# Optimization experiments

Hardware: AMD Instinct MI355X
Metric: run time of the kernel (lower is better)

Reference implementation:

```python
import jax, jax.numpy as jnp
import numpy as np

B = 32768
ONE_STEP = 344  # 12*6 + 8*6 + 18*6 + 2+2+2 + 13 + 2+2 + 2 + 1 + 36 + 36 + 6+6+6


def _info(c):
    # c: [B, 344] one history step; slice per example_extend_info layout
    b = c.shape[0]
    return dict(
        hdv=c[:, 0:72].reshape(b, 12, 6),
        cav=c[:, 72:120].reshape(b, 8, 6),
        lane=c[:, 120:228].reshape(b, 18, 6),
        bott=c[:, 228:230], road_end=c[:, 230:232], target=c[:, 232:234],
        self_=c[:, 234:247].reshape(b, 1, 13),
        dist_bott=c[:, 247:249], dist_end=c[:, 249:251],
        exe=c[:, 251:253].reshape(b, 1, 2), gen=c[:, 253:254].reshape(b, 1, 1),
    )


def _star_mask(n):
    # adj = ones; adj[1:,1:] = 0  -> ego node 0 connected to everyone
    m = jnp.zeros((n, n), bool)
    return m.at[0, :].set(True).at[:, 0].set(True)


def _gat(x, adj, Wh, a1, a2, Wo, ao1, ao2):
    # pyGAT-style dense multi-head GAT (eval mode, dropout off), returns ego node feats
    h = jnp.einsum('bnf,hfo->bhno', x, Wh)                         # [B,H,N,16]
    e = jax.nn.leaky_relu(jnp.einsum('bhno,ho->bhn', h, a1)[:, :, :, None]
                          + jnp.einsum('bhno,ho->bhn', h, a2)[:, :, None, :], 0.2)
    att = jax.nn.softmax(jnp.where(adj[None, None], e, -9e15), axis=-1)
    h = jax.nn.elu(jnp.einsum('bhnm,bhmo->bhno', att, h))          # concat-head layer
    b, H, n, o = h.shape
    x2 = h.transpose(0, 2, 1, 3).reshape(b, n, H * o)              # [B,N,48]
    ho = x2 @ Wo                                                   # [B,N,64]
    e2 = jax.nn.leaky_relu((ho @ ao1)[:, :, None] + (ho @ ao2)[:, None, :], 0.2)
    att2 = jax.nn.softmax(jnp.where(adj[None], e2, -9e15), axis=-1)
    return jax.nn.elu(jnp.einsum('bnm,bmo->bno', att2, ho))[:, 0, :]


def _fwd(obs, W_self, b_self, W_dyn, b_dyn,
         hdv_Wh, hdv_a1, hdv_a2, hdv_Wo, hdv_ao1, hdv_ao2,
         cav_Wh, cav_a1, cav_a2, cav_Wo, cav_ao1, cav_ao2,
         lane_W1, lane_b1, lane_W2, lane_b2,
         comb_W1, comb_b1, comb_W2, comb_b2):
    b = obs.shape[0]
    # history chunks: [h5,h4,h3,h2,h1,current]; forward uses h4..current
    infos = [_info(obs[:, i * ONE_STEP:(i + 1) * ONE_STEP]) for i in (1, 2, 3, 4, 5)]
    cur = infos[-1]
    ego_hist = jnp.concatenate([inf['self_'][:, :, :3] for inf in infos], axis=2)  # [B,1,15]
    x = jax.nn.leaky_relu(ego_hist @ W_self + b_self, 0.1)[:, 0, :]                # squeeze(1)
    ego_feat = jax.nn.leaky_relu(x, 0.1) @ W_dyn + b_dyn                            # [B,64]
    ego3 = cur['self_'][:, :, :3]
    hdv_rel = _gat(jnp.concatenate([ego3, cur['hdv'][:, :, :3]], axis=1), _star_mask(13),
                   hdv_Wh, hdv_a1, hdv_a2, hdv_Wo, hdv_ao1, hdv_ao2)
    cav_rel = _gat(jnp.concatenate([ego3, cur['cav'][:, :, :3]], axis=1), _star_mask(9),
                   cav_Wh, cav_a1, cav_a2, cav_Wo, cav_ao1, cav_ao2)
    lane = jax.nn.relu(jax.nn.relu(cur['lane'].reshape(b, 108) @ lane_W1 + lane_b1) @ lane_W2 + lane_b2)
    road = jnp.concatenate([cur['bott'], cur['dist_bott'], cur['road_end'],
                            cur['dist_end'], cur['target']], axis=1)               # [B,10]
    comb = jnp.concatenate([ego_feat, hdv_rel, cav_rel, lane, road,
                            cur['gen'].reshape(b, 1), cur['exe'].reshape(b, 2)], axis=1)  # [B,269]
    return jax.nn.relu(jax.nn.relu(comb @ comb_W1 + comb_b1) @ comb_W2 + comb_b2)  # [B,64]


def setup_inputs() -> dict:
    ks = jax.random.split(jax.random.key(0), 24)
    def n(i, shape):
        return jax.random.normal(ks[i], shape, jnp.float32) * 0.1
    z = lambda s: jnp.zeros(s, jnp.float32)
    return {
        'obs': jax.random.normal(ks[0], (B, 6 * ONE_STEP), jnp.float32),
        'W_self': n(1, (15, 128)), 'b_self': z((128,)),
        'W_dyn': n(2, (128, 64)), 'b_dyn': z((64,)),
        'hdv_Wh': n(3, (3, 3, 16)), 'hdv_a1': n(4, (3, 16)), 'hdv_a2': n(5, (3, 16)),
        'hdv_Wo': n(6, (48, 64)), 'hdv_ao1': n(7, (64,)), 'hdv_ao2': n(8, (64,)),
        'cav_Wh': n(9, (3, 3, 16)), 'cav_a1': n(10, (3, 16)), 'cav_a2': n(11, (3, 16)),
        'cav_Wo': n(12, (48, 64)), 'cav_ao1': n(13, (64,)), 'cav_ao2': n(14, (64,)),
        'lane_W1': n(15, (108, 64)), 'lane_b1': z((64,)),
        'lane_W2': n(16, (64, 64)), 'lane_b2': z((64,)),
        'comb_W1': n(17, (269, 64)), 'comb_b1': z((64,)),
        'comb_W2': n(18, (64, 64)), 'comb_b2': z((64,)),
        'batch_size': B,
    }


def reference(obs, W_self, b_self, W_dyn, b_dyn,
              hdv_Wh, hdv_a1, hdv_a2, hdv_Wo, hdv_ao1, hdv_ao2,
              cav_Wh, cav_a1, cav_a2, cav_Wo, cav_ao1, cav_ao2,
              lane_W1, lane_b1, lane_W2, lane_b2,
              comb_W1, comb_b1, comb_W2, comb_b2, batch_size):
    return _fwd(obs, W_self, b_self, W_dyn, b_dyn,
                hdv_Wh, hdv_a1, hdv_a2, hdv_Wo, hdv_ao1, hdv_ao2,
                cav_Wh, cav_a1, cav_a2, cav_Wo, cav_ao1, cav_ao2,
                lane_W1, lane_b1, lane_W2, lane_b2,
                comb_W1, comb_b1, comb_W2, comb_b2)
```

## Files before the change

### kernel.cpp

```cpp
#include <hip/hip_runtime.h>
#include <math.h>

#define ROW 2064
#define OS  344

typedef _Float16 h2 __attribute__((ext_vector_type(2)));
typedef _Float16 h8 __attribute__((ext_vector_type(8)));

#define OFF_EGO 0
#define OFF_DYN 3072
#define OFF_L1  11264
#define OFF_L2  18432
#define OFF_WHX 22528
#define OFF_WO  22912
#define OFF_W1  29056
#define OFF_W2  47488
#define WT_F16  51584
#define FB_BSELF 0
#define FB_BDYN 128
#define FB_LB1 192
#define FB_LB2 256
#define FB_CB1 320
#define FB_CB2 384
#define FB_SU  448
#define FB_AO  484
#define FS_TOT 740

union U4 { uint4 q; h2 p[8]; };
union U1 { uint u; h2 h; };

__device__ __forceinline__ float fd(h2 a, h2 b, float c){
#if __has_builtin(__builtin_amdgcn_fdot2)
  return __builtin_amdgcn_fdot2(a,b,c,false);
#else
  return c + (float)a.x*(float)b.x + (float)a.y*(float)b.y;
#endif
}
__device__ __forceinline__ float lrelu(float x,float s){ return x>=0.f? x : s*x; }
__device__ __forceinline__ float eluf(float x){ return x>0.f? x : expm1f(x); }
__device__ __forceinline__ uint packh2(float a,float b){ U1 u; u.h=(h2){(_Float16)a,(_Float16)b}; return u.u; }

__device__ __forceinline__ int span_to_comb(int sp){
  switch(sp){ case 228: return 256; case 229: return 257; case 230: return 260; case 231: return 261;
    case 232: return 264; case 233: return 265; case 247: return 258; case 248: return 259;
    case 249: return 262; case 250: return 263; case 251: return 267; case 252: return 268;
    case 253: return 266; default: return -1; }
}

__global__ void k_prep(const float* __restrict__ Wself, const float* __restrict__ Wdyn,
                       const float* __restrict__ lW1, const float* __restrict__ lW2,
                       const float* __restrict__ hWh, const float* __restrict__ cWh,
                       const float* __restrict__ hWo, const float* __restrict__ cWo,
                       const float* __restrict__ ha1, const float* __restrict__ ha2,
                       const float* __restrict__ ca1, const float* __restrict__ ca2,
                       const float* __restrict__ hao1, const float* __restrict__ hao2,
                       const float* __restrict__ cao1, const float* __restrict__ cao2,
                       const float* __restrict__ bself, const float* __restrict__ bdyn,
                       const float* __restrict__ lb1, const float* __restrict__ lb2,
                       const float* __restrict__ cb1, const float* __restrict__ cb2,
                       _Float16* __restrict__ wt)
{
  int gid = blockIdx.x*blockDim.x + threadIdx.x;
  int nth = gridDim.x*blockDim.x;
  for (int idx = gid; idx < OFF_W1; idx += nth){
    float v = 0.f;
    if (idx < OFF_DYN){ int l=idx; int j=l/24, k=l%24;
      if (k<16){ int s=k>>2, c=k&3; if (c<3) v = Wself[(s*3+c)*128 + j]; }
      else { int sp = 232 + (k-16); if (sp>=234 && sp<=236) v = Wself[(12+(sp-234))*128 + j]; }
    } else if (idx < OFF_L1){ int l=idx-OFF_DYN; int j=l>>7, k=l&127; v = Wdyn[k*64+j]; }
    else if (idx < OFF_L2){ int l=idx-OFF_L1; int j=l/112, k=l%112; if (k<108) v = lW1[k*64+j]; }
    else if (idx < OFF_WHX){ int l=idx-OFF_L2; int j=l>>6, k=l&63; v = lW2[k*64+j]; }
    else if (idx < OFF_WO){ int l=idx-OFF_WHX; int g=l/192; l-=g*192; int j=l>>2, k=l&3;
      const float* Wh = g? cWh : hWh; int hh=j>>4, o=j&15; if (k<3) v = Wh[hh*48 + k*16 + o]; }
    else { int l=idx-OFF_WO; int g=l/3072; l-=g*3072; int j=l/48, k=l%48;
      const float* Wo = g? cWo : hWo; v = Wo[k*64+j]; }
    wt[idx] = (_Float16)v;
  }
  float* fso = (float*)(wt + WT_F16);
  for (int i = gid; i < FS_TOT; i += nth){
    float v=0.f;
    if (i<128) v = bself[i];
    else if (i<192) v = bdyn[i-128];
    else if (i<256) v = lb1[i-192];
    else if (i<320) v = lb2[i-256];
    else if (i<384) v = cb1[i-320];
    else if (i<448) v = cb2[i-384];
    else if (i<484){ int t=i-448; int g=t/18, w=(t%18)/9, hh=(t%9)/3, f=t%3;
      const float* A = g? (w? ca2:ca1) : (w? ha2:ha1);
      const float* WH = g? cWh : hWh; v=0.f;
      for (int o=0;o<16;++o) v += WH[hh*48+f*16+o]*A[hh*16+o]; }
    else { int t=i-484; int g=t>>7, w=(t>>6)&1, j=t&63;
      const float* A = g? (w?cao2:cao1) : (w?hao2:hao1); v = A[j]; }
    fso[i]=v;
  }
}

__global__ void k_prep2(const float* __restrict__ cmW1, const float* __restrict__ cmW2,
                        _Float16* __restrict__ wt)
{
  int gid = blockIdx.x*blockDim.x + threadIdx.x;
  int nth = gridDim.x*blockDim.x;
  for (int idx = gid + OFF_W1; idx < WT_F16; idx += nth){
    float v = 0.f;
    if (idx < OFF_W2){ int l=idx-OFF_W1; int j=l/288, k=l%288;
      int r = (k<256) ? k : span_to_comb(224 + (k-256));
      if (r>=0) v = cmW1[r*64 + j];
    } else { int l=idx-OFF_W2; int j=l>>6, k=l&63; v = cmW2[k*64+j]; }
    wt[idx] = (_Float16)v;
  }
}

__device__ __forceinline__ float dot8u(uint a,uint b,uint c,uint d, const U4& q, float t){
  U1 u; u.u=a; t=fd(u.h,q.p[0],t); u.u=b; t=fd(u.h,q.p[1],t);
  u.u=c; t=fd(u.h,q.p[2],t); u.u=d; t=fd(u.h,q.p[3],t); return t;
}

__device__ __forceinline__ void gpass8(float acc[8], const _Float16* xl,
    const _Float16* __restrict__ wt, long wbase, int KP, int C){
  #pragma unroll 2
  for (int c=0;c<C;++c){
    union{h8 v; uint u[4];} x; x.v = *(const h8*)(xl + (long)c*512);
    #pragma unroll
    for (int j=0;j<8;++j){
      U4 q = *(const U4*)(wt + wbase + (long)j*KP + c*8);
      acc[j] = dot8u(x.u[0],x.u[1],x.u[2],x.u[3],q,acc[j]);
    }
  }
}

__device__ __forceinline__ void put_piece(_Float16* pbase, int wj, int lane, const float* v8){
  uint4 q; q.x=packh2(v8[0],v8[1]); q.y=packh2(v8[2],v8[3]);
  q.z=packh2(v8[4],v8[5]); q.w=packh2(v8[6],v8[7]);
  *(uint4*)(pbase + wj*512 + lane*8) = q;
}

template<int N>
__device__ __forceinline__ void gat_phase1(const float* __restrict__ fs,
    const _Float16* __restrict__ wt, const float* __restrict__ nod,
    int g, int hh, _Float16* scr, int lane)
{
  const int xoff = (N==13)? 0 : 72;
  float sx0=nod[234], sy0=nod[235], sz0=nod[236];
  float u10=fs[FB_SU+g*18+hh*3+0], u11=fs[FB_SU+g*18+hh*3+1], u12=fs[FB_SU+g*18+hh*3+2];
  float u20=fs[FB_SU+g*18+9+hh*3+0], u21=fs[FB_SU+g*18+9+hh*3+1], u22=fs[FB_SU+g*18+9+hh*3+2];
  float s1v = u10*sx0 + u11*sy0 + u12*sz0;
  float sc[N]; float mx = -1e30f;
  #pragma unroll
  for (int n=0;n<N;++n){
    float nx,ny,nz;
    if (n==0){ nx=sx0; ny=sy0; nz=sz0; }
    else { int b0=xoff+(n-1)*6; nx=nod[b0]; ny=nod[b0+1]; nz=nod[b0+2]; }
    float ev = lrelu(s1v + u20*nx + u21*ny + u22*nz, 0.2f);
    sc[n]=ev; mx=fmaxf(mx,ev);
  }
  float sum=0.f;
  #pragma unroll
  for (int n=0;n<N;++n){ float w=__expf(sc[n]-mx); sc[n]=w; sum+=w; }
  float inv = 1.f/sum;
  float g0=0.f,g1=0.f,g2=0.f;
  #pragma unroll
  for (int n=0;n<N;++n){
    float a = sc[n]*inv; float nx,ny,nz;
    if (n==0){ nx=sx0; ny=sy0; nz=sz0; }
    else { int b0=xoff+(n-1)*6; nx=nod[b0]; ny=nod[b0+1]; nz=nod[b0+2]; }
    g0 += a*nx; g1 += a*ny; g2 += a*nz;
  }
  const _Float16* wh = wt + OFF_WHX + g*192 + (hh*16)*4;
  uint o20[8], o2X[8];
  #pragma unroll
  for (int t=0;t<8;++t){
    float wa0=(float)wh[(2*t)*4],   wa1=(float)wh[(2*t)*4+1],   wa2=(float)wh[(2*t)*4+2];
    float wb0=(float)wh[(2*t+1)*4], wb1=(float)wh[(2*t+1)*4+1], wb2=(float)wh[(2*t+1)*4+2];
    float v0 = eluf(g0*wa0 + g1*wa1 + g2*wa2);
    float v1 = eluf(g0*wb0 + g1*wb1 + g2*wb2);
    float xv0= eluf(sx0*wa0 + sy0*wa1 + sz0*wa2);
    float xv1= eluf(sx0*wb0 + sy0*wb1 + sz0*wb2);
    o20[t]=packh2(v0,v1); o2X[t]=packh2(xv0,xv1);
  }
  int c20 = (g*2)*6 + 2*hh, c2X = (g*2+1)*6 + 2*hh;
  *(uint4*)(scr + (long)c20*512 + lane*8)     = make_uint4(o20[0],o20[1],o20[2],o20[3]);
  *(uint4*)(scr + (long)(c20+1)*512 + lane*8) = make_uint4(o20[4],o20[5],o20[6],o20[7]);
  *(uint4*)(scr + (long)c2X*512 + lane*8)     = make_uint4(o2X[0],o2X[1],o2X[2],o2X[3]);
  *(uint4*)(scr + (long)(c2X+1)*512 + lane*8) = make_uint4(o2X[4],o2X[5],o2X[6],o2X[7]);
}

__global__ __launch_bounds__(512,4) void k_main(const float* __restrict__ obs,
    const _Float16* __restrict__ wt, float* __restrict__ out, int Bn)
{
  __shared__ __align__(16) unsigned char smem[60416];
  _Float16* slt = (_Float16*)smem;
  _Float16* scr = (_Float16*)(smem + 17408);
  float*    pp  = (float*)(smem + 41984);
  _Float16* pbx = (_Float16*)(smem + 52224);

  const float* fs = (const float*)(wt + WT_F16);
  int wj   = __builtin_amdgcn_readfirstlane((int)(threadIdx.x >> 6));
  int lane = threadIdx.x & 63;
  int jb   = 8*wj;
  int e0   = blockIdx.x*64;
  int ge   = e0 + lane; int gec = ge < Bn ? ge : Bn-1;
  const float* nod   = obs + (long)gec*ROW + 5*OS;
  const float* myrow = obs + (long)gec*ROW;

  for (int t=wj; t<64; t+=8){
    int gx = e0 + t; if (gx >= Bn) gx = Bn-1;
    float4 v = *(const float4*)(obs + (long)gx*ROW + 5*OS + 4*lane);
    if (lane >= 30){
      uint2 w; w.x = packh2(v.x,v.y); w.y = packh2(v.z,v.w);
      *(uint2*)(slt + (long)((lane>>1)-15)*512 + t*8 + (lane&1)*4) = w;
    }
  }
  uint xe[12];
  #pragma unroll
  for (int s=0;s<4;++s){
    float2 ab = *(const float2*)(myrow + (s+1)*OS + 234);
    float2 cd = *(const float2*)(myrow + (s+1)*OS + 236);
    xe[2*s]=packh2(ab.x,ab.y); xe[2*s+1]=packh2(cd.x,cd.y);
  }
  __syncthreads();
  { union{h8 v; uint u[4];} t29; t29.v = *(const h8*)(slt + 14*512 + lane*8);
    xe[8]=t29.u[0]; xe[9]=t29.u[1]; xe[10]=t29.u[2]; xe[11]=t29.u[3]; }

  {
    uint own[8];
    #pragma unroll
    for (int p=0;p<2;++p){
      float acc[8]; int cb = 16*wj + 8*p;
      #pragma unroll
      for (int j=0;j<8;++j) acc[j] = fs[FB_BSELF + cb + j];
      #pragma unroll
      for (int c=0;c<3;++c){
        uint a=xe[4*c], b=xe[4*c+1], cc2=xe[4*c+2], d=xe[4*c+3];
        #pragma unroll
        for (int j=0;j<8;++j){
          U4 q = *(const U4*)(wt + OFF_EGO + (long)(cb+j)*24 + c*8);
          acc[j] = dot8u(a,b,cc2,d,q,acc[j]);
        }
      }
      #pragma unroll
      for (int t=0;t<4;++t){
        float a=acc[2*t], b=acc[2*t+1];
        a = a>=0.f? a : 0.01f*a;  b = b>=0.f? b : 0.01f*b;
        own[4*p+t] = packh2(a,b);
      }
    }
    *(uint4*)(scr + (long)(2*wj)*512 + lane*8)   = make_uint4(own[0],own[1],own[2],own[3]);
    *(uint4*)(scr + (long)(2*wj+1)*512 + lane*8) = make_uint4(own[4],own[5],own[6],own[7]);
  }
  __syncthreads();

  float accW1[8];
  {
    float ef[8];
    #pragma unroll
    for (int j=0;j<8;++j) ef[j] = fs[FB_BDYN + jb + j];
    gpass8(ef, scr + lane*8, wt, OFF_DYN + (long)jb*128, 128, 16);
    __syncthreads();
    put_piece(pbx, wj, lane, ef);
  }
  __syncthreads();
  #pragma unroll
  for (int j=0;j<8;++j) accW1[j] = fs[FB_CB1 + jb + j];
  gpass8(accW1, pbx + lane*8, wt, OFF_W1 + (long)jb*288, 288, 8);
  __syncthreads();

  {
    float l1[8];
    #pragma unroll
    for (int j=0;j<8;++j) l1[j] = fs[FB_LB1 + jb + j];
    gpass8(l1, slt + lane*8, wt, OFF_L1 + (long)jb*112, 112, 14);
    #pragma unroll
    for (int j=0;j<8;++j) l1[j] = fmaxf(l1[j],0.f);
    put_piece(pbx, wj, lane, l1);
  }
  __syncthreads();
  {
    float l2[8];
    #pragma unroll
    for (int j=0;j<8;++j) l2[j] = fs[FB_LB2 + jb + j];
    gpass8(l2, pbx + lane*8, wt, OFF_L2 + (long)jb*64, 64, 8);
    __syncthreads();
    #pragma unroll
    for (int j=0;j<8;++j) l2[j] = fmaxf(l2[j],0.f);
    put_piece(pbx, wj, lane, l2);
  }
  __syncthreads();
  gpass8(accW1, pbx + lane*8, wt, OFF_W1 + (long)jb*288 + 192, 288, 8);
  __syncthreads();

  if (wj < 3)             gat_phase1<13>(fs, wt, nod, 0, wj,   scr, lane);
  else if (wj>=4 && wj<7) gat_phase1<9> (fs, wt, nod, 1, wj-4, scr, lane);
  __syncthreads();

  for (int g=0; g<2; ++g){
    const int N = g? 9 : 13;
    float a0[8], aX[8];
    #pragma unroll
    for (int j=0;j<8;++j){ a0[j]=0.f; aX[j]=0.f; }
    long wb = OFF_WO + g*3072 + (long)jb*48;
    #pragma unroll 2
    for (int c=0;c<6;++c){
      union{h8 v; uint u[4];} x0, x1;
      x0.v = *(const h8*)(scr + (long)((g*2)*6+c)*512 + lane*8);
      x1.v = *(const h8*)(scr + (long)((g*2+1)*6+c)*512 + lane*8);
      #pragma unroll
      for (int j=0;j<8;++j){
        U4 q = *(const U4*)(wt + wb + (long)j*48 + c*8);
        a0[j] = dot8u(x0.u[0],x0.u[1],x0.u[2],x0.u[3],q,a0[j]);
        aX[j] = dot8u(x1.u[0],x1.u[1],x1.u[2],x1.u[3],q,aX[j]);
      }
    }
    float p1=0.f,p2=0.f,p3=0.f;
    #pragma unroll
    for (int j=0;j<8;++j){
      float w1v=fs[FB_AO + g*128 + jb + j], w2v=fs[FB_AO + g*128 + 64 + jb + j];
      p1 += a0[j]*w1v; p2 += a0[j]*w2v; p3 += aX[j]*w2v;
    }
    { float* pr = pp + (long)(wj*64+lane)*5; pr[0]=p1; pr[1]=p2; pr[2]=p3; }
    __syncthreads();
    float q1=0.f,q2=0.f,q3=0.f;
    #pragma unroll
    for (int w=0;w<8;++w){ const float* pr = pp + (long)(w*64+lane)*5;
      q1+=pr[0]; q2+=pr[1]; q3+=pr[2]; }
    float e00=lrelu(q1+q2,0.2f), e0X=lrelu(q1+q3,0.2f);
    float mm=fmaxf(e00,e0X);
    float w0=__expf(e00-mm), wX=__expf(e0X-mm);
    float invden = 1.f/(w0 + (float)(N-1)*wX);
    float kX = (float)(N-1)*wX*invden; w0 *= invden;
    float og[8];
    #pragma unroll
    for (int j=0;j<8;++j) og[j] = eluf(w0*a0[j] + kX*aX[j]);
    put_piece(pbx, wj, lane, og);
    __syncthreads();
    gpass8(accW1, pbx + lane*8, wt, OFF_W1 + (long)jb*288 + 64 + 64*g, 288, 8);
    __syncthreads();
  }

  gpass8(accW1, slt + 13*512 + lane*8, wt, OFF_W1 + (long)jb*288 + 256, 288, 4);

  {
    float ch[8];
    #pragma unroll
    for (int j=0;j<8;++j) ch[j] = fmaxf(accW1[j],0.f);
    put_piece(pbx, wj, lane, ch);
  }
  __syncthreads();
  {
    float o[8];
    #pragma unroll
    for (int j=0;j<8;++j) o[j] = fs[FB_CB2 + jb + j];
    gpass8(o, pbx + lane*8, wt, OFF_W2 + (long)jb*64, 64, 8);
    if (ge < Bn){
      float4 v0, v1;
      v0.x=fmaxf(o[0],0.f); v0.y=fmaxf(o[1],0.f); v0.z=fmaxf(o[2],0.f); v0.w=fmaxf(o[3],0.f);
      v1.x=fmaxf(o[4],0.f); v1.y=fmaxf(o[5],0.f); v1.z=fmaxf(o[6],0.f); v1.w=fmaxf(o[7],0.f);
      *(float4*)(out + (long)ge*64 + jb)     = v0;
      *(float4*)(out + (long)ge*64 + jb + 4) = v1;
    }
  }
}

extern "C" void kernel_launch(void* const* d_in, const int* in_sizes, int n_in,
                              void* d_out, int out_size, void* d_ws, size_t ws_size,
                              hipStream_t stream)
{
  const float* obs  =(const float*)d_in[0];
  const float* Wself=(const float*)d_in[1];  const float* bself=(const float*)d_in[2];
  const float* Wdyn =(const float*)d_in[3];  const float* bdyn =(const float*)d_in[4];
  const float* hWh  =(const float*)d_in[5];  const float* ha1  =(const float*)d_in[6];
  const float* ha2  =(const float*)d_in[7];  const float* hWo  =(const float*)d_in[8];
  const float* hao1 =(const float*)d_in[9];  const float* hao2 =(const float*)d_in[10];
  const float* cWh  =(const float*)d_in[11]; const float* ca1  =(const float*)d_in[12];
  const float* ca2  =(const float*)d_in[13]; const float* cWo  =(const float*)d_in[14];
  const float* cao1 =(const float*)d_in[15]; const float* cao2 =(const float*)d_in[16];
  const float* lW1  =(const float*)d_in[17]; const float* lb1  =(const float*)d_in[18];
  const float* lW2  =(const float*)d_in[19]; const float* lb2  =(const float*)d_in[20];
  const float* cmW1 =(const float*)d_in[21]; const float* cmb1 =(const float*)d_in[22];
  const float* cmW2 =(const float*)d_in[23]; const float* cmb2 =(const float*)d_in[24];

  int Bn = in_sizes[0] / ROW;
  _Float16* wt = (_Float16*)d_ws;
  float* out = (float*)d_out;

  k_prep<<<64,256,0,stream>>>(Wself,Wdyn,lW1,lW2,hWh,cWh,hWo,cWo,ha1,ha2,ca1,ca2,
                              hao1,hao2,cao1,cao2,bself,bdyn,lb1,lb2,cmb1,cmb2,wt);
  k_prep2<<<64,256,0,stream>>>(cmW1,cmW2,wt);
  int blocks = (Bn + 63)/64;
  k_main<<<blocks,512,0,stream>>>(obs,wt,out,Bn);
}
```

Baseline: 418.6 us.

## Merge prep kernels, drop barriers, fuse GAT softmax pass, hoist ego loads

Merges the two weight-prep kernels into one launch with a larger grid, which saves a kernel launch. Two __syncthreads calls in the main kernel are removed. The GAT phase-1 softmax now preloads node coordinates into registers and folds the normalisation into the weighted sum, saving one loop. The ego history loads are hoisted ahead of the tile-loading loop, and ELU uses __expf(x)-1 in place of expm1f. Removing the barriers risks races on shared scratch buffers if another warp still reads the buffer being overwritten, and __expf-1 loses precision near zero.

```diff
diff --git a/kernel.cpp b/kernel.cpp
--- a/kernel.cpp
+++ b/kernel.cpp
@@ -37,7 +37,7 @@
 #endif
 }
 __device__ __forceinline__ float lrelu(float x,float s){ return x>=0.f? x : s*x; }
-__device__ __forceinline__ float eluf(float x){ return x>0.f? x : expm1f(x); }
+__device__ __forceinline__ float eluf(float x){ return x>0.f? x : __expf(x)-1.f; }
 __device__ __forceinline__ uint packh2(float a,float b){ U1 u; u.h=(h2){(_Float16)a,(_Float16)b}; return u.u; }
 
 __device__ __forceinline__ int span_to_comb(int sp){
@@ -47,7 +47,7 @@
     case 253: return 266; default: return -1; }
 }
 
-__global__ void k_prep(const float* __restrict__ Wself, const float* __restrict__ Wdyn,
+__global__ void k_prep_all(const float* __restrict__ Wself, const float* __restrict__ Wdyn,
                        const float* __restrict__ lW1, const float* __restrict__ lW2,
                        const float* __restrict__ hWh, const float* __restrict__ cWh,
                        const float* __restrict__ hWo, const float* __restrict__ cWo,
@@ -58,11 +58,12 @@
                        const float* __restrict__ bself, const float* __restrict__ bdyn,
                        const float* __restrict__ lb1, const float* __restrict__ lb2,
                        const float* __restrict__ cb1, const float* __restrict__ cb2,
+                       const float* __restrict__ cmW1, const float* __restrict__ cmW2,
                        _Float16* __restrict__ wt)
 {
   int gid = blockIdx.x*blockDim.x + threadIdx.x;
   int nth = gridDim.x*blockDim.x;
-  for (int idx = gid; idx < OFF_W1; idx += nth){
+  for (int idx = gid; idx < WT_F16; idx += nth){
     float v = 0.f;
     if (idx < OFF_DYN){ int l=idx; int j=l/24, k=l%24;
       if (k<16){ int s=k>>2, c=k&3; if (c<3) v = Wself[(s*3+c)*128 + j]; }
@@ -72,8 +73,12 @@
     else if (idx < OFF_WHX){ int l=idx-OFF_L2; int j=l>>6, k=l&63; v = lW2[k*64+j]; }
     else if (idx < OFF_WO){ int l=idx-OFF_WHX; int g=l/192; l-=g*192; int j=l>>2, k=l&3;
       const float* Wh = g? cWh : hWh; int hh=j>>4, o=j&15; if (k<3) v = Wh[hh*48 + k*16 + o]; }
-    else { int l=idx-OFF_WO; int g=l/3072; l-=g*3072; int j=l/48, k=l%48;
+    else if (idx < OFF_W1){ int l=idx-OFF_WO; int g=l/3072; l-=g*3072; int j=l/48, k=l%48;
       const float* Wo = g? cWo : hWo; v = Wo[k*64+j]; }
+    else if (idx < OFF_W2){ int l=idx-OFF_W1; int j=l/288, k=l%288;
+      int r = (k<256) ? k : span_to_comb(224 + (k-256));
+      if (r>=0) v = cmW1[r*64 + j];
+    } else { int l=idx-OFF_W2; int j=l>>6, k=l&63; v = cmW2[k*64+j]; }
     wt[idx] = (_Float16)v;
   }
   float* fso = (float*)(wt + WT_F16);
@@ -95,21 +100,6 @@
   }
 }
 
-__global__ void k_prep2(const float* __restrict__ cmW1, const float* __restrict__ cmW2,
-                        _Float16* __restrict__ wt)
-{
-  int gid = blockIdx.x*blockDim.x + threadIdx.x;
-  int nth = gridDim.x*blockDim.x;
-  for (int idx = gid + OFF_W1; idx < WT_F16; idx += nth){
-    float v = 0.f;
-    if (idx < OFF_W2){ int l=idx-OFF_W1; int j=l/288, k=l%288;
-      int r = (k<256) ? k : span_to_comb(224 + (k-256));
-      if (r>=0) v = cmW1[r*64 + j];
-    } else { int l=idx-OFF_W2; int j=l>>6, k=l&63; v = cmW2[k*64+j]; }
-    wt[idx] = (_Float16)v;
-  }
-}
-
 __device__ __forceinline__ float dot8u(uint a,uint b,uint c,uint d, const U4& q, float t){
   U1 u; u.u=a; t=fd(u.h,q.p[0],t); u.u=b; t=fd(u.h,q.p[1],t);
   u.u=c; t=fd(u.h,q.p[2],t); u.u=d; t=fd(u.h,q.p[3],t); return t;
@@ -140,31 +130,27 @@
     int g, int hh, _Float16* scr, int lane)
 {
   const int xoff = (N==13)? 0 : 72;
-  float sx0=nod[234], sy0=nod[235], sz0=nod[236];
   float u10=fs[FB_SU+g*18+hh*3+0], u11=fs[FB_SU+g*18+hh*3+1], u12=fs[FB_SU+g*18+hh*3+2];
   float u20=fs[FB_SU+g*18+9+hh*3+0], u21=fs[FB_SU+g*18+9+hh*3+1], u22=fs[FB_SU+g*18+9+hh*3+2];
+  float px[N], py[N], pz[N];
+  px[0]=nod[234]; py[0]=nod[235]; pz[0]=nod[236];
+  #pragma unroll
+  for (int n=1;n<N;++n){ int b0=xoff+(n-1)*6; px[n]=nod[b0]; py[n]=nod[b0+1]; pz[n]=nod[b0+2]; }
+  float sx0=px[0], sy0=py[0], sz0=pz[0];
   float s1v = u10*sx0 + u11*sy0 + u12*sz0;
   float sc[N]; float mx = -1e30f;
   #pragma unroll
   for (int n=0;n<N;++n){
-    float nx,ny,nz;
-    if (n==0){ nx=sx0; ny=sy0; nz=sz0; }
-    else { int b0=xoff+(n-1)*6; nx=nod[b0]; ny=nod[b0+1]; nz=nod[b0+2]; }
-    float ev = lrelu(s1v + u20*nx + u21*ny + u22*nz, 0.2f);
+    float ev = lrelu(s1v + u20*px[n] + u21*py[n] + u22*pz[n], 0.2f);
     sc[n]=ev; mx=fmaxf(mx,ev);
   }
-  float sum=0.f;
-  #pragma unroll
-  for (int n=0;n<N;++n){ float w=__expf(sc[n]-mx); sc[n]=w; sum+=w; }
-  float inv = 1.f/sum;
-  float g0=0.f,g1=0.f,g2=0.f;
+  float sum=0.f, g0=0.f, g1=0.f, g2=0.f;
   #pragma unroll
   for (int n=0;n<N;++n){
-    float a = sc[n]*inv; float nx,ny,nz;
-    if (n==0){ nx=sx0; ny=sy0; nz=sz0; }
-    else { int b0=xoff+(n-1)*6; nx=nod[b0]; ny=nod[b0+1]; nz=nod[b0+2]; }
-    g0 += a*nx; g1 += a*ny; g2 += a*nz;
-  }
+    float w=__expf(sc[n]-mx); sum+=w;
+    g0 += w*px[n]; g1 += w*py[n]; g2 += w*pz[n];
+  }
+  float inv = 1.f/sum; g0*=inv; g1*=inv; g2*=inv;
   const _Float16* wh = wt + OFF_WHX + g*192 + (hh*16)*4;
   uint o20[8], o2X[8];
   #pragma unroll
@@ -202,6 +188,14 @@
   const float* nod   = obs + (long)gec*ROW + 5*OS;
   const float* myrow = obs + (long)gec*ROW;
 
+  float2 ha[4], hb[4];
+  #pragma unroll
+  for (int s=0;s<4;++s){
+    ha[s] = *(const float2*)(myrow + (s+1)*OS + 234);
+    hb[s] = *(const float2*)(myrow + (s+1)*OS + 236);
+  }
+
+  #pragma unroll
   for (int t=wj; t<64; t+=8){
     int gx = e0 + t; if (gx >= Bn) gx = Bn-1;
     float4 v = *(const float4*)(obs + (long)gx*ROW + 5*OS + 4*lane);
@@ -212,11 +206,7 @@
   }
   uint xe[12];
   #pragma unroll
-  for (int s=0;s<4;++s){
-    float2 ab = *(const float2*)(myrow + (s+1)*OS + 234);
-    float2 cd = *(const float2*)(myrow + (s+1)*OS + 236);
-    xe[2*s]=packh2(ab.x,ab.y); xe[2*s+1]=packh2(cd.x,cd.y);
-  }
+  for (int s=0;s<4;++s){ xe[2*s]=packh2(ha[s].x,ha[s].y); xe[2*s+1]=packh2(hb[s].x,hb[s].y); }
   __syncthreads();
   { union{h8 v; uint u[4];} t29; t29.v = *(const h8*)(slt + 14*512 + lane*8);
     xe[8]=t29.u[0]; xe[9]=t29.u[1]; xe[10]=t29.u[2]; xe[11]=t29.u[3]; }
@@ -255,7 +245,6 @@
     #pragma unroll
     for (int j=0;j<8;++j) ef[j] = fs[FB_BDYN + jb + j];
     gpass8(ef, scr + lane*8, wt, OFF_DYN + (long)jb*128, 128, 16);
-    __syncthreads();
     put_piece(pbx, wj, lane, ef);
   }
   __syncthreads();
@@ -286,7 +275,6 @@
   }
   __syncthreads();
   gpass8(accW1, pbx + lane*8, wt, OFF_W1 + (long)jb*288 + 192, 288, 8);
-  __syncthreads();
 
   if (wj < 3)             gat_phase1<13>(fs, wt, nod, 0, wj,   scr, lane);
   else if (wj>=4 && wj<7) gat_phase1<9> (fs, wt, nod, 1, wj-4, scr, lane);
@@ -382,9 +370,9 @@
   _Float16* wt = (_Float16*)d_ws;
   float* out = (float*)d_out;
 
-  k_prep<<<64,256,0,stream>>>(Wself,Wdyn,lW1,lW2,hWh,cWh,hWo,cWo,ha1,ha2,ca1,ca2,
-                              hao1,hao2,cao1,cao2,bself,bdyn,lb1,lb2,cmb1,cmb2,wt);
-  k_prep2<<<64,256,0,stream>>>(cmW1,cmW2,wt);
+  k_prep_all<<<128,256,0,stream>>>(Wself,Wdyn,lW1,lW2,hWh,cWh,hWo,cWo,ha1,ha2,ca1,ca2,
+                                   hao1,hao2,cao1,cao2,bself,bdyn,lb1,lb2,cmb1,cmb2,
+                                   cmW1,cmW2,wt);
   int blocks = (Bn + 63)/64;
   k_main<<<blocks,512,0,stream>>>(obs,wt,out,Bn);
 }
```

Result: faster. 408.8 us (-2.3%).
